# Kernel optimization log

Measured on AMD Instinct MI355X. Metric: run time of the kernel, lower is better.

The kernel has to match this reference:

```python
import jax, jax.numpy as jnp
import numpy as np

EPS = 1e-5  # BatchNorm1d default eps


def _xavier_uniform(key, shape):
    # torch xavier: fan_in = shape[1]*prod(shape[2:]), fan_out = shape[0]*prod(shape[2:])
    rf = int(np.prod(shape[2:])) if len(shape) > 2 else 1
    fan_in = shape[1] * rf
    fan_out = shape[0] * rf
    bound = float(np.sqrt(6.0 / (fan_in + fan_out)))
    return jax.random.uniform(key, shape, jnp.float32, -bound, bound)


def setup_inputs() -> dict:
    key = jax.random.key(0)
    ks = jax.random.split(key, 6)
    d_in, h1, h2, d_out = 256, 512, 512, 256
    B = 4096
    x = jax.random.normal(ks[0], (B, 1, d_in), dtype=jnp.float32)
    W1 = _xavier_uniform(ks[1], (h1, d_in))
    b1 = jnp.zeros((h1,), jnp.float32)
    gamma = jnp.ones((1, 1, 1), jnp.float32)   # BatchNorm1d(1) weight
    beta = jnp.zeros((1, 1, 1), jnp.float32)   # BatchNorm1d(1) bias
    coeffs2 = _xavier_uniform(ks[2], (2, h2, h1, 16))
    bias2 = jnp.zeros((1, h2), jnp.float32)
    coeffs3 = _xavier_uniform(ks[3], (2, d_out, h2, 8))
    bias3 = jnp.zeros((1, d_out), jnp.float32)
    return {"x": x, "W1": W1, "b1": b1, "gamma": gamma, "beta": beta,
            "coeffs2": coeffs2, "bias2": bias2, "coeffs3": coeffs3, "bias3": bias3}


def _fourier_kan(x, coeffs, bias, gridsize):
    # x: (N, in)  coeffs: (2, out, in, grid)  ->  (N, out)
    k = jnp.arange(1, gridsize + 1, dtype=x.dtype)          # (grid,)
    arg = x[:, :, None] * k                                  # (N, in, grid) -- basis computed ONCE
    y = jnp.einsum('nig,oig->no', jnp.cos(arg), coeffs[0])
    y = y + jnp.einsum('nig,oig->no', jnp.sin(arg), coeffs[1])
    return y + bias


def reference(x, W1, b1, gamma, beta, coeffs2, bias2, coeffs3, bias3):
    # x: (B, 1, d_in)
    h = jnp.einsum('bcd,hd->bch', x, W1) + b1                # Linear -> (B,1,h1)
    # BatchNorm1d(1), training-mode batch stats over (N, L) for the single channel
    mean = jnp.mean(h, axis=(0, 2), keepdims=True)
    var = jnp.mean((h - mean) ** 2, axis=(0, 2), keepdims=True)
    h = gamma * (h - mean) * jax.lax.rsqrt(var + EPS) + beta
    h = jax.nn.relu(h)
    h = h.reshape(-1, h.shape[-1])                           # (B, h1)
    h = _fourier_kan(h, coeffs2, bias2, 16)                  # (B, h2)
    h = _fourier_kan(h, coeffs3, bias3, 8)                   # (B, out)
    return jax.nn.softmax(h, axis=1)
```

## Files before the change

kernel.cpp:

```cpp
#include <hip/hip_runtime.h>
#include <hip/hip_fp16.h>
#include <stdint.h>

typedef unsigned short u16;
typedef unsigned int u32;
typedef long i64;
typedef short bf16x8 __attribute__((ext_vector_type(8)));
typedef float f32x4 __attribute__((ext_vector_type(4)));

#define SCALE_C   1024.f
#define INV_SCALE 0.0009765625f

__device__ __forceinline__ float bf2f(u16 v) { return __uint_as_float(((u32)v) << 16); }

__device__ __forceinline__ u16 f2bf(float a) {
  u32 u = __float_as_uint(a); u += 0x7FFFu + ((u >> 16) & 1u); return (u16)(u >> 16);
}

__device__ __forceinline__ u32 packbf2(float a, float b) {
  u32 ua = __float_as_uint(a); ua += 0x7FFFu + ((ua >> 16) & 1u);
  u32 ub = __float_as_uint(b); ub += 0x7FFFu + ((ub >> 16) & 1u);
  return (ua >> 16) | (ub & 0xFFFF0000u);
}

__device__ __forceinline__ u32 packfp8x4(float a, float b, float c, float d) {
  u32 lo = (u32)__builtin_amdgcn_cvt_pk_fp8_f32(a, b, 0, false);
  return (u32)__builtin_amdgcn_cvt_pk_fp8_f32(c, d, (int)lo, true);
}

__device__ __forceinline__ float inval(const void* p, int idx, int isf) {
  return isf ? ((const float*)p)[idx] : bf2f(((const u16*)p)[idx]);
}

__device__ __forceinline__ void split_body(
    const void* __restrict__ src, u16* __restrict__ dst, int i, int isf, int lo_pos)
{
  int row = i >> 6, g = i & 63;
  float v[4];
  if (isf) {
    float4 t = ((const float4*)src)[i];
    v[0] = t.x; v[1] = t.y; v[2] = t.z; v[3] = t.w;
  } else {
    uint2 t = ((const uint2*)src)[i];
    const u16* p = (const u16*)&t;
    v[0] = bf2f(p[0]); v[1] = bf2f(p[1]); v[2] = bf2f(p[2]); v[3] = bf2f(p[3]);
  }
  u16 hi[4]; float lo[4];
  #pragma unroll
  for (int j = 0; j < 4; ++j) { hi[j] = f2bf(v[j]); lo[j] = v[j] - bf2f(hi[j]); }
  u32 hw0 = (u32)hi[0] | ((u32)hi[1] << 16);
  u32 hw1 = (u32)hi[2] | ((u32)hi[3] << 16);
  u32 lw0 = packbf2(lo[0], lo[1]);
  u32 lw1 = packbf2(lo[2], lo[3]);
  u32* base = (u32*)(dst + (size_t)row * 768);
  int c = g * 2;
  base[c] = hw0; base[c + 1] = hw1;
  if (lo_pos == 1) {
    base[128 + c] = lw0; base[128 + c + 1] = lw1;
    base[256 + c] = hw0; base[256 + c + 1] = hw1;
  } else {
    base[128 + c] = hw0; base[128 + c + 1] = hw1;
    base[256 + c] = lw0; base[256 + c + 1] = lw1;
  }
}

__global__ __launch_bounds__(256) void prep_all_kernel(
    const void* __restrict__ x, const void* __restrict__ W1,
    u16* __restrict__ Xs, u16* __restrict__ W1s,
    const void* __restrict__ c2, unsigned char* __restrict__ w2f8,
    const void* __restrict__ c3, unsigned char* __restrict__ w3f8,
    int* __restrict__ flag)
{
  __shared__ int sf[4];
  const int t = threadIdx.x, wave = t >> 6;
  {
    float v = fabsf(bf2f(((const u16*)W1)[t & 127]));
    int bad = !(v < 1e6f);
    unsigned long long b = __ballot(bad);
    if ((t & 63) == 0) sf[wave] = (b != 0ull) ? 1 : 0;
  }
  __syncthreads();
  const int isf = sf[0] | sf[1] | sf[2] | sf[3];
  const int bid = blockIdx.x;
  if (bid == 0 && t == 0) *flag = isf;
  if (bid < 1024) {
    split_body(x, Xs, bid * 256 + t, isf, 1);
  } else if (bid < 1152) {
    split_body(W1, W1s, (bid - 1024) * 256 + t, isf, 2);
  } else if (bid < 2176) {
    int u = (bid - 1152) * 256 + t;
    int o = u >> 9, i = u & 511;
    u32* d = (u32*)(w2f8 + (size_t)o * 16384 + i * 32);
    if (isf) {
      const float4* f0 = (const float4*)((const float*)c2 + ((size_t)o * 512 + i) * 16);
      const float4* f1 = (const float4*)((const float*)c2 + (size_t)512 * 512 * 16 + ((size_t)o * 512 + i) * 16);
      #pragma unroll
      for (int j = 0; j < 4; ++j) { float4 v = f0[j]; d[j]   = packfp8x4(v.x*SCALE_C, v.y*SCALE_C, v.z*SCALE_C, v.w*SCALE_C); }
      #pragma unroll
      for (int j = 0; j < 4; ++j) { float4 v = f1[j]; d[4+j] = packfp8x4(v.x*SCALE_C, v.y*SCALE_C, v.z*SCALE_C, v.w*SCALE_C); }
    } else {
      const u16* s0 = (const u16*)c2 + ((size_t)o * 512 + i) * 16;
      const u16* s1 = (const u16*)c2 + (size_t)512 * 512 * 16 + ((size_t)o * 512 + i) * 16;
      #pragma unroll
      for (int j = 0; j < 4; ++j) d[j]   = packfp8x4(bf2f(s0[4*j])*SCALE_C, bf2f(s0[4*j+1])*SCALE_C, bf2f(s0[4*j+2])*SCALE_C, bf2f(s0[4*j+3])*SCALE_C);
      #pragma unroll
      for (int j = 0; j < 4; ++j) d[4+j] = packfp8x4(bf2f(s1[4*j])*SCALE_C, bf2f(s1[4*j+1])*SCALE_C, bf2f(s1[4*j+2])*SCALE_C, bf2f(s1[4*j+3])*SCALE_C);
    }
  } else {
    int u = (bid - 2176) * 256 + t;
    int o = u >> 9, i = u & 511;
    u32* d = (u32*)(w3f8 + (size_t)o * 8192 + i * 16);
    if (isf) {
      const float4* f0 = (const float4*)((const float*)c3 + ((size_t)o * 512 + i) * 8);
      const float4* f1 = (const float4*)((const float*)c3 + (size_t)256 * 512 * 8 + ((size_t)o * 512 + i) * 8);
      #pragma unroll
      for (int j = 0; j < 2; ++j) { float4 v = f0[j]; d[j]   = packfp8x4(v.x*SCALE_C, v.y*SCALE_C, v.z*SCALE_C, v.w*SCALE_C); }
      #pragma unroll
      for (int j = 0; j < 2; ++j) { float4 v = f1[j]; d[2+j] = packfp8x4(v.x*SCALE_C, v.y*SCALE_C, v.z*SCALE_C, v.w*SCALE_C); }
    } else {
      const u16* s0 = (const u16*)c3 + ((size_t)o * 512 + i) * 8;
      const u16* s1 = (const u16*)c3 + (size_t)256 * 512 * 8 + ((size_t)o * 512 + i) * 8;
      #pragma unroll
      for (int j = 0; j < 2; ++j) d[j]   = packfp8x4(bf2f(s0[4*j])*SCALE_C, bf2f(s0[4*j+1])*SCALE_C, bf2f(s0[4*j+2])*SCALE_C, bf2f(s0[4*j+3])*SCALE_C);
      #pragma unroll
      for (int j = 0; j < 2; ++j) d[2+j] = packfp8x4(bf2f(s1[4*j])*SCALE_C, bf2f(s1[4*j+1])*SCALE_C, bf2f(s1[4*j+2])*SCALE_C, bf2f(s1[4*j+3])*SCALE_C);
    }
  }
}

#define L1_LD 136
__global__ __launch_bounds__(256) void l1_kernel(
    const u16* __restrict__ xs, const u16* __restrict__ w1s, const void* __restrict__ b1,
    const int* __restrict__ flag, float* __restrict__ H, float2* __restrict__ PT)
{
  __shared__ u16 sA[128 * L1_LD];
  __shared__ u16 sB[64 * L1_LD];
  __shared__ float redbuf[8];
  const int n0 = blockIdx.x * 128, o0 = blockIdx.y * 64;
  const int t = threadIdx.x, wave = t >> 6, lane = t & 63, quad = lane >> 4, l16 = lane & 15;
  const int isf = *flag;
  f32x4 acc[2][4] = {};
  for (int ks = 0; ks < 768; ks += 128) {
    #pragma unroll
    for (int r = 0; r < 8; ++r) {
      int idx = t + r * 256;
      int row = idx >> 4, col = idx & 15;
      const uint4* src = (const uint4*)(xs + (size_t)(n0 + row) * 768 + ks) + col;
      *(uint4*)&sA[row * L1_LD + col * 8] = *src;
    }
    #pragma unroll
    for (int r = 0; r < 4; ++r) {
      int idx = t + r * 256;
      int row = idx >> 4, col = idx & 15;
      const uint4* src = (const uint4*)(w1s + (size_t)(o0 + row) * 768 + ks) + col;
      *(uint4*)&sB[row * L1_LD + col * 8] = *src;
    }
    __syncthreads();
    #pragma unroll
    for (int kk = 0; kk < 128; kk += 32) {
      bf16x8 bfr[4];
      #pragma unroll
      for (int fo = 0; fo < 4; ++fo)
        bfr[fo] = *(const bf16x8*)&sB[(fo * 16 + l16) * L1_LD + kk + quad * 8];
      #pragma unroll
      for (int fm = 0; fm < 2; ++fm) {
        bf16x8 av = *(const bf16x8*)&sA[(wave * 32 + fm * 16 + l16) * L1_LD + kk + quad * 8];
        #pragma unroll
        for (int fo = 0; fo < 4; ++fo)
          acc[fm][fo] = __builtin_amdgcn_mfma_f32_16x16x32_bf16(av, bfr[fo], acc[fm][fo], 0, 0, 0);
      }
    }
    __syncthreads();
  }
  float s = 0.f, sq = 0.f;
  #pragma unroll
  for (int fm = 0; fm < 2; ++fm)
  #pragma unroll
  for (int fo = 0; fo < 4; ++fo) {
    int o = o0 + fo * 16 + l16;
    float bias = inval(b1, o, isf);
    #pragma unroll
    for (int r = 0; r < 4; ++r) {
      int n = n0 + wave * 32 + fm * 16 + quad * 4 + r;
      float h = acc[fm][fo][r] + bias;
      H[(size_t)n * 512 + o] = h;
      s += h; sq += h * h;
    }
  }
  #pragma unroll
  for (int off = 32; off; off >>= 1) { s += __shfl_down(s, off); sq += __shfl_down(sq, off); }
  if (lane == 0) { redbuf[wave] = s; redbuf[4 + wave] = sq; }
  __syncthreads();
  if (t == 0) {
    float S = redbuf[0] + redbuf[1] + redbuf[2] + redbuf[3];
    float Q = redbuf[4] + redbuf[5] + redbuf[6] + redbuf[7];
    PT[blockIdx.y * 32 + blockIdx.x] = make_float2(S, Q);
  }
}

__global__ __launch_bounds__(256) void red_kernel(const float2* __restrict__ PT, float* __restrict__ ST)
{
  __shared__ float sa[4], sb[4];
  const int t = threadIdx.x;
  float2 p = PT[t];
  float s = p.x, q = p.y;
  #pragma unroll
  for (int off = 32; off; off >>= 1) { s += __shfl_down(s, off); q += __shfl_down(q, off); }
  if ((t & 63) == 0) { sa[t >> 6] = s; sb[t >> 6] = q; }
  __syncthreads();
  if (t == 0) {
    float S = sa[0] + sa[1] + sa[2] + sa[3];
    float Q = sb[0] + sb[1] + sb[2] + sb[3];
    const float N = 4096.f * 512.f;
    float mean = S / N;
    float var = Q / N - mean * mean;
    ST[0] = mean;
    ST[1] = rsqrtf(var + 1e-5f);
  }
}

#define K2_LDB 144
__global__ __launch_bounds__(256) void kan2_kernel(
    const float* __restrict__ H, const unsigned char* __restrict__ w2f8,
    const void* __restrict__ gammap, const void* __restrict__ betap,
    const int* __restrict__ flag, const float* __restrict__ ST,
    float* __restrict__ P, int kzT)
{
  __shared__ unsigned char sA8[64 * K2_LDB];
  __shared__ unsigned char sB8[128 * K2_LDB];
  const int n0 = blockIdx.x * 64, o0 = blockIdx.y * 128, kz = blockIdx.z;
  const int t = threadIdx.x, wave = t >> 6, lane = t & 63, quad = lane >> 4, l16 = lane & 15;
  const int wm = (wave & 1) * 32, wo = (wave >> 1) * 64;
  const int isf = *flag;
  const float mean = ST[0];
  const float gs = inval(gammap, 0, isf) * ST[1];
  const float beta = inval(betap, 0, isf);
  const int am = t >> 2, ai = t & 3;
  const int q = 128 / kzT, rr = 128 % kzT;
  const int nst = q + (kz < rr ? 1 : 0);
  const int i0 = (kz * q + (kz < rr ? kz : rr)) * 4;
  const int r0 = t >> 3, seg = t & 7;
  const unsigned char* bsrc = w2f8 + (size_t)(o0 + r0) * 16384 + (size_t)i0 * 32 + seg * 16;
  const float* hsrc = H + (size_t)(n0 + am) * 512 + i0 + ai;
  f32x4 acc[2][4] = {};
  float ph = *hsrc;
  for (int s = 0; s < nst; ++s) {
    #pragma unroll
    for (int p = 0; p < 4; ++p) {
      uint4 v = *(const uint4*)(bsrc + (size_t)p * 32 * 16384);
      *(uint4*)&sB8[(r0 + 32 * p) * K2_LDB + seg * 16] = v;
    }
    {
      float a = fmaxf((ph - mean) * gs + beta, 0.f);
      float s1, c1; __sincosf(a, &s1, &c1);
      float t2 = c1 + c1;
      float cg[16], sg[16];
      cg[0] = c1; sg[0] = s1;
      cg[1] = fmaf(t2, c1, -1.f); sg[1] = t2 * s1;
      #pragma unroll
      for (int g = 2; g < 16; ++g) {
        cg[g] = fmaf(t2, cg[g-1], -cg[g-2]);
        sg[g] = fmaf(t2, sg[g-1], -sg[g-2]);
      }
      u32 pk[8];
      #pragma unroll
      for (int j = 0; j < 4; ++j) pk[j]   = packfp8x4(cg[4*j], cg[4*j+1], cg[4*j+2], cg[4*j+3]);
      #pragma unroll
      for (int j = 0; j < 4; ++j) pk[4+j] = packfp8x4(sg[4*j], sg[4*j+1], sg[4*j+2], sg[4*j+3]);
      uint4* dst = (uint4*)&sA8[am * K2_LDB + ai * 32];
      dst[0] = *(uint4*)&pk[0]; dst[1] = *(uint4*)&pk[4];
    }
    __syncthreads();
    bsrc += 128; hsrc += 4;
    if (s + 1 < nst) ph = *hsrc;
    #pragma unroll
    for (int kk = 0; kk < 128; kk += 32) {
      i64 bfr[4], afr[2];
      #pragma unroll
      for (int fo = 0; fo < 4; ++fo)
        bfr[fo] = *(const i64*)&sB8[(wo + fo * 16 + l16) * K2_LDB + kk + quad * 8];
      #pragma unroll
      for (int fm = 0; fm < 2; ++fm)
        afr[fm] = *(const i64*)&sA8[(wm + fm * 16 + l16) * K2_LDB + kk + quad * 8];
      #pragma unroll
      for (int fm = 0; fm < 2; ++fm)
      #pragma unroll
      for (int fo = 0; fo < 4; ++fo)
        acc[fm][fo] = __builtin_amdgcn_mfma_f32_16x16x32_fp8_fp8(afr[fm], bfr[fo], acc[fm][fo], 0, 0, 0);
    }
    __syncthreads();
  }
  float* Pk = P + (size_t)kz * (4096 * 512);
  #pragma unroll
  for (int fm = 0; fm < 2; ++fm)
  #pragma unroll
  for (int fo = 0; fo < 4; ++fo) {
    int o = o0 + wo + fo * 16 + l16;
    #pragma unroll
    for (int r = 0; r < 4; ++r) {
      int n = n0 + wm + fm * 16 + quad * 4 + r;
      Pk[(size_t)n * 512 + o] = acc[fm][fo][r] * INV_SCALE;
    }
  }
}

__global__ __launch_bounds__(256) void reduce2_kernel(
    const float* __restrict__ P, const void* __restrict__ bias2,
    const int* __restrict__ flag, float* __restrict__ H2, int kzT)
{
  int i = blockIdx.x * 256 + threadIdx.x;
  const int isf = *flag;
  float4 a = ((const float4*)P)[i];
  float rx = a.x, ry = a.y, rz = a.z, rw = a.w;
  for (int k = 1; k < kzT; ++k) {
    float4 b = ((const float4*)(P + (size_t)k * 4096 * 512))[i];
    rx += b.x; ry += b.y; rz += b.z; rw += b.w;
  }
  int o = (i * 4) & 511;
  float4 r;
  r.x = rx + inval(bias2, o + 0, isf);
  r.y = ry + inval(bias2, o + 1, isf);
  r.z = rz + inval(bias2, o + 2, isf);
  r.w = rw + inval(bias2, o + 3, isf);
  ((float4*)H2)[i] = r;
}

#define K3_LDB 144
__global__ __launch_bounds__(256) void kan3_kernel(
    const float* __restrict__ H2, const unsigned char* __restrict__ w3f8,
    const int* __restrict__ flag, float* __restrict__ Q)
{
  __shared__ unsigned char sA8[32 * K3_LDB];
  __shared__ unsigned char sB8[128 * K3_LDB];
  const int n0 = blockIdx.x * 32, o0 = blockIdx.y * 128, kz = blockIdx.z;
  const int t = threadIdx.x, wave = t >> 6, lane = t & 63, quad = lane >> 4, l16 = lane & 15;
  const int wo = wave * 32;
  const int am = t >> 3, ai = t & 7;
  const int nst = 10 + (kz < 4 ? 1 : 0);
  const int i0 = (kz * 10 + (kz < 4 ? kz : 4)) * 8;
  const int r0 = t >> 3, seg = t & 7;
  const unsigned char* bsrc = w3f8 + (size_t)(o0 + r0) * 8192 + (size_t)i0 * 16 + seg * 16;
  const float* hsrc = H2 + (size_t)(n0 + am) * 512 + i0 + ai;
  f32x4 acc[2][2] = {};
  float ph = *hsrc;
  for (int s = 0; s < nst; ++s) {
    #pragma unroll
    for (int p = 0; p < 4; ++p) {
      uint4 v = *(const uint4*)(bsrc + (size_t)p * 32 * 8192);
      *(uint4*)&sB8[(r0 + 32 * p) * K3_LDB + seg * 16] = v;
    }
    {
      float s1, c1; __sincosf(ph, &s1, &c1);
      float t2 = c1 + c1;
      float cg[8], sg[8];
      cg[0] = c1; sg[0] = s1;
      cg[1] = fmaf(t2, c1, -1.f); sg[1] = t2 * s1;
      #pragma unroll
      for (int g = 2; g < 8; ++g) {
        cg[g] = fmaf(t2, cg[g-1], -cg[g-2]);
        sg[g] = fmaf(t2, sg[g-1], -sg[g-2]);
      }
      u32 pk[4];
      pk[0] = packfp8x4(cg[0], cg[1], cg[2], cg[3]);
      pk[1] = packfp8x4(cg[4], cg[5], cg[6], cg[7]);
      pk[2] = packfp8x4(sg[0], sg[1], sg[2], sg[3]);
      pk[3] = packfp8x4(sg[4], sg[5], sg[6], sg[7]);
      *(uint4*)&sA8[am * K3_LDB + ai * 16] = *(uint4*)&pk[0];
    }
    __syncthreads();
    bsrc += 128; hsrc += 8;
    if (s + 1 < nst) ph = *hsrc;
    #pragma unroll
    for (int kk = 0; kk < 128; kk += 32) {
      i64 bfr[2], afr[2];
      #pragma unroll
      for (int fo = 0; fo < 2; ++fo)
        bfr[fo] = *(const i64*)&sB8[(wo + fo * 16 + l16) * K3_LDB + kk + quad * 8];
      #pragma unroll
      for (int fm = 0; fm < 2; ++fm)
        afr[fm] = *(const i64*)&sA8[(fm * 16 + l16) * K3_LDB + kk + quad * 8];
      #pragma unroll
      for (int fm = 0; fm < 2; ++fm)
      #pragma unroll
      for (int fo = 0; fo < 2; ++fo)
        acc[fm][fo] = __builtin_amdgcn_mfma_f32_16x16x32_fp8_fp8(afr[fm], bfr[fo], acc[fm][fo], 0, 0, 0);
    }
    __syncthreads();
  }
  float* Qk = Q + (size_t)kz * (4096 * 256);
  #pragma unroll
  for (int fm = 0; fm < 2; ++fm)
  #pragma unroll
  for (int fo = 0; fo < 2; ++fo) {
    int o = o0 + wo + fo * 16 + l16;
    #pragma unroll
    for (int r = 0; r < 4; ++r) {
      int n = n0 + fm * 16 + quad * 4 + r;
      Qk[(size_t)n * 256 + o] = acc[fm][fo][r] * INV_SCALE;
    }
  }
}

__global__ __launch_bounds__(256) void softmax_kernel(
    const float* __restrict__ Q, const void* __restrict__ bias3,
    const int* __restrict__ flag, float* __restrict__ out)
{
  const int t = threadIdx.x, wave = t >> 6, lane = t & 63;
  const int row = blockIdx.x * 4 + wave;
  const int isf = *flag;
  size_t base = (size_t)row * 256 + lane * 4;
  float v0 = 0.f, v1 = 0.f, v2 = 0.f, v3 = 0.f;
  #pragma unroll
  for (int k = 0; k < 6; ++k) {
    float4 a = *(const float4*)(Q + (size_t)k * 4096 * 256 + base);
    v0 += a.x; v1 += a.y; v2 += a.z; v3 += a.w;
  }
  int o = lane * 4;
  v0 += inval(bias3, o + 0, isf);
  v1 += inval(bias3, o + 1, isf);
  v2 += inval(bias3, o + 2, isf);
  v3 += inval(bias3, o + 3, isf);
  float m = fmaxf(fmaxf(v0, v1), fmaxf(v2, v3));
  #pragma unroll
  for (int off = 32; off; off >>= 1) m = fmaxf(m, __shfl_xor(m, off));
  float e0 = __expf(v0 - m), e1 = __expf(v1 - m), e2 = __expf(v2 - m), e3 = __expf(v3 - m);
  float s = e0 + e1 + e2 + e3;
  #pragma unroll
  for (int off = 32; off; off >>= 1) s += __shfl_xor(s, off);
  float inv = 1.f / s;
  *(float4*)(out + base) = make_float4(e0 * inv, e1 * inv, e2 * inv, e3 * inv);
}

extern "C" void kernel_launch(void* const* d_in, const int* in_sizes, int n_in,
                              void* d_out, int out_size, void* d_ws, size_t ws_size,
                              hipStream_t stream)
{
  const void* x     = d_in[0];
  const void* W1    = d_in[1];
  const void* b1    = d_in[2];
  const void* gamma = d_in[3];
  const void* beta  = d_in[4];
  const void* c2    = d_in[5];
  const void* bias2 = d_in[6];
  const void* c3    = d_in[7];
  const void* bias3 = d_in[8];

  const int kz2 = (ws_size >= (75ull << 20)) ? 5 : 3;

  char* ws = (char*)d_ws;
  float*          H    = (float*)(ws + 0);
  float*          H2   = (float*)(ws + (8ull  << 20));
  unsigned char*  W2F8 = (unsigned char*)(ws + (16ull << 20));
  unsigned char*  W3F8 = (unsigned char*)(ws + (24ull << 20));
  u16*            Xs   = (u16*)(ws + (26ull << 20));
  u16*            W1s  = (u16*)(ws + (33ull << 20));
  float*          P2   = (float*)(ws + (34ull << 20));
  float*          Q3   = (float*)(ws + (34ull << 20));
  size_t tail = (kz2 == 5) ? ((74ull << 20) + 524288) : (58ull << 20);
  float2* PT   = (float2*)(ws + tail);
  float*  STT  = (float*) (ws + tail + 65536);
  int*    FLAG = (int*)   (ws + tail + 131072);

  prep_all_kernel<<<dim3(2688), dim3(256), 0, stream>>>(x, W1, Xs, W1s, c2, W2F8, c3, W3F8, FLAG);
  l1_kernel   <<<dim3(32, 8), dim3(256), 0, stream>>>(Xs, W1s, b1, FLAG, H, PT);
  red_kernel  <<<dim3(1),    dim3(256), 0, stream>>>(PT, STT);
  kan2_kernel <<<dim3(64, 4, kz2), dim3(256), 0, stream>>>(H, W2F8, gamma, beta, FLAG, STT, P2, kz2);
  reduce2_kernel<<<dim3(2048), dim3(256), 0, stream>>>(P2, bias2, FLAG, H2, kz2);
  kan3_kernel <<<dim3(128, 2, 6), dim3(256), 0, stream>>>(H2, W3F8, FLAG, Q3);
  softmax_kernel<<<dim3(1024), dim3(256), 0, stream>>>(Q3, bias3, FLAG, (float*)d_out);
}
```

Baseline: 230.5 us.

## Fuse batch-norm stat reduction into kan2 and split-K reduce into kan3

Removes the single-block red_kernel by having every kan2 block reduce the 256 per-tile partial sums itself to compute mean and rstd. Also removes reduce2_kernel: kan3 now sums the kz2 split-K partial buffers plus bias2 directly when loading each activation. This cuts two launches and the H2 write/read round trip. In exchange, each kan3 block rereads kz2 partial values per element, redundantly across its o-tiles and kz slices, and the reads now sit on the load path inside the main loop.

Result: no change. 227.6 us (-1.2%).

```diff
diff --git a/kernel.cpp b/kernel.cpp
--- a/kernel.cpp
+++ b/kernel.cpp
@@ -198,42 +198,34 @@
   }
 }
 
-__global__ __launch_bounds__(256) void red_kernel(const float2* __restrict__ PT, float* __restrict__ ST)
-{
-  __shared__ float sa[4], sb[4];
-  const int t = threadIdx.x;
-  float2 p = PT[t];
-  float s = p.x, q = p.y;
-  #pragma unroll
-  for (int off = 32; off; off >>= 1) { s += __shfl_down(s, off); q += __shfl_down(q, off); }
-  if ((t & 63) == 0) { sa[t >> 6] = s; sb[t >> 6] = q; }
-  __syncthreads();
-  if (t == 0) {
-    float S = sa[0] + sa[1] + sa[2] + sa[3];
-    float Q = sb[0] + sb[1] + sb[2] + sb[3];
-    const float N = 4096.f * 512.f;
-    float mean = S / N;
-    float var = Q / N - mean * mean;
-    ST[0] = mean;
-    ST[1] = rsqrtf(var + 1e-5f);
-  }
-}
-
 #define K2_LDB 144
 __global__ __launch_bounds__(256) void kan2_kernel(
     const float* __restrict__ H, const unsigned char* __restrict__ w2f8,
     const void* __restrict__ gammap, const void* __restrict__ betap,
-    const int* __restrict__ flag, const float* __restrict__ ST,
+    const int* __restrict__ flag, const float2* __restrict__ PT,
     float* __restrict__ P, int kzT)
 {
   __shared__ unsigned char sA8[64 * K2_LDB];
   __shared__ unsigned char sB8[128 * K2_LDB];
+  __shared__ float sred[8];
   const int n0 = blockIdx.x * 64, o0 = blockIdx.y * 128, kz = blockIdx.z;
   const int t = threadIdx.x, wave = t >> 6, lane = t & 63, quad = lane >> 4, l16 = lane & 15;
   const int wm = (wave & 1) * 32, wo = (wave >> 1) * 64;
   const int isf = *flag;
-  const float mean = ST[0];
-  const float gs = inval(gammap, 0, isf) * ST[1];
+  {
+    float2 p = PT[t];
+    float s = p.x, q = p.y;
+    #pragma unroll
+    for (int off = 32; off; off >>= 1) { s += __shfl_down(s, off); q += __shfl_down(q, off); }
+    if (lane == 0) { sred[wave] = s; sred[4 + wave] = q; }
+  }
+  __syncthreads();
+  const float Ssum = sred[0] + sred[1] + sred[2] + sred[3];
+  const float Qsum = sred[4] + sred[5] + sred[6] + sred[7];
+  const float Nn = 4096.f * 512.f;
+  const float mean = Ssum / Nn;
+  const float rstd = rsqrtf(Qsum / Nn - mean * mean + 1e-5f);
+  const float gs = inval(gammap, 0, isf) * rstd;
   const float beta = inval(betap, 0, isf);
   const int am = t >> 2, ai = t & 3;
   const int q = 128 / kzT, rr = 128 % kzT;
@@ -304,31 +296,11 @@
   }
 }
 
-__global__ __launch_bounds__(256) void reduce2_kernel(
-    const float* __restrict__ P, const void* __restrict__ bias2,
-    const int* __restrict__ flag, float* __restrict__ H2, int kzT)
-{
-  int i = blockIdx.x * 256 + threadIdx.x;
-  const int isf = *flag;
-  float4 a = ((const float4*)P)[i];
-  float rx = a.x, ry = a.y, rz = a.z, rw = a.w;
-  for (int k = 1; k < kzT; ++k) {
-    float4 b = ((const float4*)(P + (size_t)k * 4096 * 512))[i];
-    rx += b.x; ry += b.y; rz += b.z; rw += b.w;
-  }
-  int o = (i * 4) & 511;
-  float4 r;
-  r.x = rx + inval(bias2, o + 0, isf);
-  r.y = ry + inval(bias2, o + 1, isf);
-  r.z = rz + inval(bias2, o + 2, isf);
-  r.w = rw + inval(bias2, o + 3, isf);
-  ((float4*)H2)[i] = r;
-}
-
 #define K3_LDB 144
 __global__ __launch_bounds__(256) void kan3_kernel(
-    const float* __restrict__ H2, const unsigned char* __restrict__ w3f8,
-    const int* __restrict__ flag, float* __restrict__ Q)
+    const float* __restrict__ P2, const void* __restrict__ bias2,
+    const unsigned char* __restrict__ w3f8,
+    const int* __restrict__ flag, float* __restrict__ Q, int kzT2)
 {
   __shared__ unsigned char sA8[32 * K3_LDB];
   __shared__ unsigned char sB8[128 * K3_LDB];
@@ -339,10 +311,16 @@
   const int nst = 10 + (kz < 4 ? 1 : 0);
   const int i0 = (kz * 10 + (kz < 4 ? kz : 4)) * 8;
   const int r0 = t >> 3, seg = t & 7;
+  const int isf = *flag;
   const unsigned char* bsrc = w3f8 + (size_t)(o0 + r0) * 8192 + (size_t)i0 * 16 + seg * 16;
-  const float* hsrc = H2 + (size_t)(n0 + am) * 512 + i0 + ai;
+  const float* psrc = P2 + (size_t)(n0 + am) * 512 + i0 + ai;
   f32x4 acc[2][2] = {};
-  float ph = *hsrc;
+  float ph;
+  {
+    float v = inval(bias2, i0 + ai, isf);
+    for (int k = 0; k < kzT2; ++k) v += psrc[(size_t)k * 4096 * 512];
+    ph = v;
+  }
   for (int s = 0; s < nst; ++s) {
     #pragma unroll
     for (int p = 0; p < 4; ++p) {
@@ -368,8 +346,12 @@
       *(uint4*)&sA8[am * K3_LDB + ai * 16] = *(uint4*)&pk[0];
     }
     __syncthreads();
-    bsrc += 128; hsrc += 8;
-    if (s + 1 < nst) ph = *hsrc;
+    bsrc += 128; psrc += 8;
+    if (s + 1 < nst) {
+      float v = inval(bias2, i0 + (s + 1) * 8 + ai, isf);
+      for (int k = 0; k < kzT2; ++k) v += psrc[(size_t)k * 4096 * 512];
+      ph = v;
+    }
     #pragma unroll
     for (int kk = 0; kk < 128; kk += 32) {
       i64 bfr[2], afr[2];
@@ -449,23 +431,19 @@
 
   char* ws = (char*)d_ws;
   float*          H    = (float*)(ws + 0);
-  float*          H2   = (float*)(ws + (8ull  << 20));
   unsigned char*  W2F8 = (unsigned char*)(ws + (16ull << 20));
   unsigned char*  W3F8 = (unsigned char*)(ws + (24ull << 20));
   u16*            Xs   = (u16*)(ws + (26ull << 20));
   u16*            W1s  = (u16*)(ws + (33ull << 20));
   float*          P2   = (float*)(ws + (34ull << 20));
-  float*          Q3   = (float*)(ws + (34ull << 20));
-  size_t tail = (kz2 == 5) ? ((74ull << 20) + 524288) : (58ull << 20);
+  float*          Q3   = (float*)(ws + 0);
+  size_t tail = (34ull << 20) + (size_t)kz2 * (8ull << 20) + 524288;
   float2* PT   = (float2*)(ws + tail);
-  float*  STT  = (float*) (ws + tail + 65536);
-  int*    FLAG = (int*)   (ws + tail + 131072);
+  int*    FLAG = (int*)   (ws + tail + 65536);
 
   prep_all_kernel<<<dim3(2688), dim3(256), 0, stream>>>(x, W1, Xs, W1s, c2, W2F8, c3, W3F8, FLAG);
   l1_kernel   <<<dim3(32, 8), dim3(256), 0, stream>>>(Xs, W1s, b1, FLAG, H, PT);
-  red_kernel  <<<dim3(1),    dim3(256), 0, stream>>>(PT, STT);
-  kan2_kernel <<<dim3(64, 4, kz2), dim3(256), 0, stream>>>(H, W2F8, gamma, beta, FLAG, STT, P2, kz2);
-  reduce2_kernel<<<dim3(2048), dim3(256), 0, stream>>>(P2, bias2, FLAG, H2, kz2);
-  kan3_kernel <<<dim3(128, 2, 6), dim3(256), 0, stream>>>(H2, W3F8, FLAG, Q3);
+  kan2_kernel <<<dim3(64, 4, kz2), dim3(256), 0, stream>>>(H, W2F8, gamma, beta, FLAG, PT, P2, kz2);
+  kan3_kernel <<<dim3(128, 2, 6), dim3(256), 0, stream>>>(P2, bias2, W3F8, FLAG, Q3, kz2);
   softmax_kernel<<<dim3(1024), dim3(256), 0, stream>>>(Q3, bias3, FLAG, (float*)d_out);
 }
```
